# Performance work log

Measured on AMD Instinct MI355X. Metric: run time of the kernel, lower is better.

Reference implementation:

```python
import math
import jax, jax.numpy as jnp
import numpy as np

QUERY_DIM = 768
FEAT_DIM = 1024
HID_DIM = 768
OUT_DIM = 768
B, L, S, T = 32, 256, 64, 64


def _linear_params(key, fan_in, fan_out):
    kw, kb = jax.random.split(key)
    scale = 1.0 / math.sqrt(fan_in)
    W = jax.random.uniform(kw, (fan_in, fan_out), jnp.float32, -scale, scale)
    b = jax.random.uniform(kb, (fan_out,), jnp.float32, -scale, scale)
    return W, b


def setup_inputs() -> dict:
    key = jax.random.key(0)
    ks = jax.random.split(key, 7)
    query = jax.random.normal(ks[0], (B, L, QUERY_DIM), jnp.float32)
    src = jax.random.normal(ks[1], (B, S, FEAT_DIM), jnp.float32)
    trg = jax.random.normal(ks[2], (B, T, FEAT_DIM), jnp.float32)
    Wq, b_q = _linear_params(ks[3], QUERY_DIM, HID_DIM)
    Ws, b_s = _linear_params(ks[4], FEAT_DIM, HID_DIM)
    Wt, b_t = _linear_params(ks[5], FEAT_DIM, HID_DIM)
    Wo, b_o = _linear_params(ks[6], HID_DIM + QUERY_DIM, OUT_DIM)
    return {"query": query, "src": src, "trg": trg,
            "Wq": Wq, "b_q": b_q, "Ws": Ws, "b_s": b_s,
            "Wt": Wt, "b_t": b_t, "Wo": Wo, "b_o": b_o}


def reference(query, src, trg, Wq, b_q, Ws, b_s, Wt, b_t, Wo, b_o):
    # Projections (LinearAct with identity activation).
    q = query @ Wq + b_q          # (b, l, h)
    s_key = src @ Ws + b_s        # (b, s, h)
    t_key = trg @ Wt + b_t        # (b, t, h)
    # rel_key[b, t, s, h] = tanh(s_key[b, s, h] + t_key[b, t, h])
    rel_key = jnp.tanh(s_key[:, None, :, :] + t_key[:, :, None, :])  # (b, t, s, h)
    # Scores over combined (t, s) positions.
    weight = jnp.einsum('blk,btsk->blts', q, rel_key) / math.sqrt(HID_DIM)  # (b, l, t, s)
    b_, l_, t_, s_ = weight.shape
    weight = jax.nn.softmax(weight.reshape(b_, l_, t_ * s_), axis=-1).reshape(b_, l_, t_, s_)
    # Context: weighted sum of rel_key over (t, s).
    rel_ctx = jnp.einsum('blts,btsk->blk', weight, rel_key)  # (b, l, h)
    x = jnp.concatenate([query, rel_ctx], axis=-1)           # (b, l, h + q)
    return jax.nn.relu(x @ Wo + b_o)                          # (b, l, out)
```

## Files before the change

kernel.cpp:

```cpp
#include <hip/hip_runtime.h>
#include <math.h>


typedef __attribute__((ext_vector_type(8))) short bf16x8;
typedef __attribute__((ext_vector_type(4))) float f32x4;

__device__ __forceinline__ unsigned short f2bf(float f) {
    union { float f; unsigned u; } x; x.f = f;
    unsigned u = x.u;
    return (unsigned short)((u + 0x7fffu + ((u >> 16) & 1u)) >> 16);
}
__device__ __forceinline__ float bf2f(unsigned short h) {
    union { unsigned u; float f; } x; x.u = (unsigned)h << 16;
    return x.f;
}
__device__ __forceinline__ float tanh_fast(float x) {
    float e = __expf(2.0f * x);
    return 1.0f - 2.0f * __builtin_amdgcn_rcpf(1.0f + e);
}
__device__ __forceinline__ void async_copy16(void* lds, const void* g) {
    __builtin_amdgcn_global_load_lds(
        (const __attribute__((address_space(1))) unsigned int*)g,
        (__attribute__((address_space(3))) unsigned int*)lds,
        16, 0, 0);
}

template<bool OUT_BF16, bool RELU>
__global__ __launch_bounds__(256, 2) void gemm_bt_kernel(
    const unsigned short* __restrict__ A, const unsigned short* __restrict__ BT,
    void* __restrict__ Cout, const float* __restrict__ bias,
    int M, int N, int K, int lda, int ldb, int ldc)
{
    __shared__ unsigned short As[128 * 32];
    __shared__ unsigned short Bs[128 * 32];
    const int m0 = blockIdx.x * 128, n0 = blockIdx.y * 128;
    const int tid = threadIdx.x;
    const int lane = tid & 63, wid = tid >> 6;
    const int wr = wid >> 1, wc = wid & 1;
    const int r = lane & 15, g = lane >> 4;

    f32x4 acc[4][4] = {};

    for (int k0 = 0; k0 < K; k0 += 32) {
        __syncthreads();
        #pragma unroll
        for (int j = 0; j < 2; ++j) {
            int c = j * 256 + tid;
            int row = c >> 2, kc = (c & 3) * 8;
            async_copy16(&As[c * 8], A  + (size_t)(m0 + row) * lda + k0 + kc);
            async_copy16(&Bs[c * 8], BT + (size_t)(n0 + row) * ldb + k0 + kc);
        }
        asm volatile("s_waitcnt vmcnt(0)" ::: "memory");
        __syncthreads();

        bf16x8 af[4], bfr[4];
        #pragma unroll
        for (int m = 0; m < 4; ++m)
            af[m] = *(const bf16x8*)&As[(wr * 64 + m * 16 + r) * 32 + g * 8];
        #pragma unroll
        for (int n = 0; n < 4; ++n)
            bfr[n] = *(const bf16x8*)&Bs[(wc * 64 + n * 16 + r) * 32 + g * 8];
        #pragma unroll
        for (int m = 0; m < 4; ++m)
            #pragma unroll
            for (int n = 0; n < 4; ++n)
                acc[m][n] = __builtin_amdgcn_mfma_f32_16x16x32_bf16(
                    af[m], bfr[n], acc[m][n], 0, 0, 0);
    }

    float* Cf = (float*)Cout;
    unsigned short* Cb = (unsigned short*)Cout;
    #pragma unroll
    for (int n = 0; n < 4; ++n) {
        int col = n0 + wc * 64 + n * 16 + r;
        float bv = bias ? bias[col] : 0.0f;
        #pragma unroll
        for (int m = 0; m < 4; ++m) {
            int row0 = m0 + wr * 64 + m * 16 + g * 4;
            #pragma unroll
            for (int i = 0; i < 4; ++i) {
                float v = acc[m][n][i] + bv;
                if (RELU) v = fmaxf(v, 0.0f);
                size_t off = (size_t)(row0 + i) * ldc + col;
                if (OUT_BF16) Cb[off] = f2bf(v);
                else          Cf[off] = v;
            }
        }
    }
}

__global__ __launch_bounds__(256, 2) void scores_kernel(
    const unsigned short* __restrict__ qh,
    const float* __restrict__ s_key,
    const float* __restrict__ t_key,
    unsigned short* __restrict__ scores)
{
    __shared__ unsigned short As[128 * 32];
    __shared__ unsigned short Bs[128 * 32];
    __shared__ float Sk[64 * 32];
    __shared__ float Tk[64];

    const int b = blockIdx.z;
    const unsigned short* A = qh + (size_t)b * 256 * 768;
    const float* skp = s_key + (size_t)b * 64 * 768;
    const float* tkp = t_key + (size_t)b * 64 * 768;
    const int m0 = blockIdx.x * 128, n0 = blockIdx.y * 128;
    const int t0 = n0 >> 6;
    const int tid = threadIdx.x;
    const int lane = tid & 63, wid = tid >> 6;
    const int wr = wid >> 1, wc = wid & 1;
    const int r = lane & 15, g = lane >> 4;

    f32x4 acc[4][4] = {};

    for (int k0 = 0; k0 < 768; k0 += 32) {
        __syncthreads();
        if (tid < 64) Tk[tid] = tkp[(size_t)(t0 + (tid >> 5)) * 768 + k0 + (tid & 31)];
        #pragma unroll
        for (int j = 0; j < 2; ++j) {
            int c = j * 256 + tid;
            int row = c >> 2, kc = (c & 3) * 8;
            async_copy16(&As[c * 8], A + (size_t)(m0 + row) * 768 + k0 + kc);
            int s = c >> 3, k4 = (c & 7) * 4;
            async_copy16(&Sk[s * 32 + k4], skp + (size_t)s * 768 + k0 + k4);
        }
        asm volatile("s_waitcnt vmcnt(0)" ::: "memory");
        __syncthreads();

        #pragma unroll
        for (int j = 0; j < 2; ++j) {
            int c = j * 256 + tid;
            int n = c >> 2, kc = (c & 3) * 8;
            const float* sv = &Sk[(n & 63) * 32 + kc];
            const float* tv = &Tk[(n >> 6) * 32 + kc];
            bf16x8 o;
            #pragma unroll
            for (int e = 0; e < 8; ++e)
                o[e] = (short)f2bf(tanh_fast(sv[e] + tv[e]));
            *(bf16x8*)&Bs[n * 32 + kc] = o;
        }
        __syncthreads();

        bf16x8 af[4], bfr[4];
        #pragma unroll
        for (int m = 0; m < 4; ++m)
            af[m] = *(const bf16x8*)&As[(wr * 64 + m * 16 + r) * 32 + g * 8];
        #pragma unroll
        for (int n = 0; n < 4; ++n)
            bfr[n] = *(const bf16x8*)&Bs[(wc * 64 + n * 16 + r) * 32 + g * 8];
        #pragma unroll
        for (int m = 0; m < 4; ++m)
            #pragma unroll
            for (int n = 0; n < 4; ++n)
                acc[m][n] = __builtin_amdgcn_mfma_f32_16x16x32_bf16(
                    af[m], bfr[n], acc[m][n], 0, 0, 0);
    }

    unsigned short* C = scores + (size_t)b * 256 * 4096;
    #pragma unroll
    for (int n = 0; n < 4; ++n) {
        int col = n0 + wc * 64 + n * 16 + r;
        #pragma unroll
        for (int m = 0; m < 4; ++m) {
            int row0 = m0 + wr * 64 + m * 16 + g * 4;
            #pragma unroll
            for (int i = 0; i < 4; ++i)
                C[(size_t)(row0 + i) * 4096 + col] = f2bf(acc[m][n][i]);
        }
    }
}

__global__ __launch_bounds__(256, 2) void ctx_kernel(
    const unsigned short* __restrict__ w,
    const float* __restrict__ s_keyT,
    const float* __restrict__ t_keyT,
    unsigned short* __restrict__ xcat)
{
    __shared__ unsigned short As[128 * 32];
    __shared__ unsigned short Bs[128 * 32];
    __shared__ float SkT[128 * 32];
    __shared__ unsigned short TkTb[128 * 64];

    const int b = blockIdx.z;
    const unsigned short* A = w + (size_t)b * 256 * 4096;
    const float* skT = s_keyT + (size_t)b * 768 * 64;
    const float* tkT = t_keyT + (size_t)b * 768 * 64;
    const int m0 = blockIdx.x * 128, n0 = blockIdx.y * 128;
    const int tid = threadIdx.x;
    const int lane = tid & 63, wid = tid >> 6;
    const int wr = wid >> 1, wc = wid & 1;
    const int r = lane & 15, g = lane >> 4;

    for (int j = tid; j < 128 * 64; j += 256)
        TkTb[j] = f2bf(tkT[(size_t)n0 * 64 + j]);

    f32x4 acc[4][4] = {};

    for (int k0 = 0; k0 < 4096; k0 += 32) {
        const int t = k0 >> 6, s0 = k0 & 63;
        __syncthreads();
        #pragma unroll
        for (int j = 0; j < 2; ++j) {
            int c = j * 256 + tid;
            int row = c >> 2, kc = (c & 3) * 8;
            async_copy16(&As[c * 8], A + (size_t)(m0 + row) * 4096 + k0 + kc);
        }
        #pragma unroll
        for (int j = 0; j < 4; ++j) {
            int c = j * 256 + tid;
            int h = c >> 3, k4 = (c & 7) * 4;
            async_copy16(&SkT[h * 32 + k4], skT + (size_t)(n0 + h) * 64 + s0 + k4);
        }
        asm volatile("s_waitcnt vmcnt(0)" ::: "memory");
        __syncthreads();

        #pragma unroll
        for (int j = 0; j < 2; ++j) {
            int c = j * 256 + tid;
            int h = c >> 2, kc = (c & 3) * 8;
            const float* sv = &SkT[h * 32 + kc];
            float tval = bf2f(TkTb[h * 64 + t]);
            bf16x8 o;
            #pragma unroll
            for (int e = 0; e < 8; ++e)
                o[e] = (short)f2bf(tanh_fast(sv[e] + tval));
            *(bf16x8*)&Bs[h * 32 + kc] = o;
        }
        __syncthreads();

        bf16x8 af[4], bfr[4];
        #pragma unroll
        for (int m = 0; m < 4; ++m)
            af[m] = *(const bf16x8*)&As[(wr * 64 + m * 16 + r) * 32 + g * 8];
        #pragma unroll
        for (int n = 0; n < 4; ++n)
            bfr[n] = *(const bf16x8*)&Bs[(wc * 64 + n * 16 + r) * 32 + g * 8];
        #pragma unroll
        for (int m = 0; m < 4; ++m)
            #pragma unroll
            for (int n = 0; n < 4; ++n)
                acc[m][n] = __builtin_amdgcn_mfma_f32_16x16x32_bf16(
                    af[m], bfr[n], acc[m][n], 0, 0, 0);
    }

    unsigned short* C = xcat + (size_t)b * 256 * 1536 + 768;
    #pragma unroll
    for (int n = 0; n < 4; ++n) {
        int col = n0 + wc * 64 + n * 16 + r;
        #pragma unroll
        for (int m = 0; m < 4; ++m) {
            int row0 = m0 + wr * 64 + m * 16 + g * 4;
            #pragma unroll
            for (int i = 0; i < 4; ++i)
                C[(size_t)(row0 + i) * 1536 + col] = f2bf(acc[m][n][i]);
        }
    }
}

__global__ void cvt_bf16_kernel(const float* __restrict__ in,
                                unsigned short* __restrict__ out, int n4) {
    int i = blockIdx.x * 256 + threadIdx.x;
    if (i >= n4) return;
    float4 v = ((const float4*)in)[i];
    ushort4 o;
    o.x = f2bf(v.x); o.y = f2bf(v.y); o.z = f2bf(v.z); o.w = f2bf(v.w);
    ((ushort4*)out)[i] = o;
}

__global__ void cvt_query_kernel(const float* __restrict__ in,
                                 unsigned short* __restrict__ xcat) {
    int i = blockIdx.x * 256 + threadIdx.x;
    if (i >= 8192 * 192) return;
    int row = i / 192, c4 = (i % 192) * 4;
    float4 v = ((const float4*)in)[i];
    ushort4 o;
    o.x = f2bf(v.x); o.y = f2bf(v.y); o.z = f2bf(v.z); o.w = f2bf(v.w);
    *(ushort4*)&xcat[(size_t)row * 1536 + c4] = o;
}

__global__ void transpose_w_kernel(const float* __restrict__ in,
                                   unsigned short* __restrict__ out,
                                   int R, int C) {
    __shared__ float tile[64][65];
    const int r0 = blockIdx.y * 64, c0 = blockIdx.x * 64;
    const int tx = threadIdx.x & 63, ty = threadIdx.x >> 6;
    for (int i = ty; i < 64; i += 4)
        tile[i][tx] = in[(size_t)(r0 + i) * C + c0 + tx];
    __syncthreads();
    for (int i = ty; i < 64; i += 4)
        out[(size_t)(c0 + i) * R + r0 + tx] = f2bf(tile[tx][i]);
}

__global__ void transpose_sk_kernel(const float* __restrict__ in,
                                    float* __restrict__ out) {
    __shared__ float tile[64][65];
    const int b = blockIdx.y, c0 = blockIdx.x * 64;
    const float* src = in + (size_t)b * 64 * 768;
    float* dst = out + (size_t)b * 768 * 64;
    const int tx = threadIdx.x & 63, ty = threadIdx.x >> 6;
    for (int i = ty; i < 64; i += 4)
        tile[i][tx] = src[(size_t)i * 768 + c0 + tx];
    __syncthreads();
    for (int i = ty; i < 64; i += 4)
        dst[(size_t)(c0 + i) * 64 + tx] = tile[tx][i];
}

__global__ __launch_bounds__(256) void softmax_kernel(unsigned short* __restrict__ scores) {
    unsigned short* p = scores + (size_t)blockIdx.x * 4096;
    const int tid = threadIdx.x, lane = tid & 63, wid = tid >> 6;
    __shared__ float red[4];

    float v[16];
    {
        const bf16x8* p8 = (const bf16x8*)p;
        bf16x8 a = p8[tid * 2], c = p8[tid * 2 + 1];
        #pragma unroll
        for (int e = 0; e < 8; ++e) {
            v[e]     = bf2f((unsigned short)a[e]);
            v[8 + e] = bf2f((unsigned short)c[e]);
        }
    }
    float mx = v[0];
    #pragma unroll
    for (int e = 1; e < 16; ++e) mx = fmaxf(mx, v[e]);
    #pragma unroll
    for (int o = 32; o; o >>= 1) mx = fmaxf(mx, __shfl_xor(mx, o));
    if (lane == 0) red[wid] = mx;
    __syncthreads();
    mx = fmaxf(fmaxf(red[0], red[1]), fmaxf(red[2], red[3]));
    __syncthreads();

    const float scale = 0.03608439182435161f;
    float sum = 0.0f;
    #pragma unroll
    for (int e = 0; e < 16; ++e) {
        v[e] = __expf((v[e] - mx) * scale);
        sum += v[e];
    }
    #pragma unroll
    for (int o = 32; o; o >>= 1) sum += __shfl_xor(sum, o);
    if (lane == 0) red[wid] = sum;
    __syncthreads();
    sum = red[0] + red[1] + red[2] + red[3];
    const float inv = 1.0f / sum;

    bf16x8* p8 = (bf16x8*)p;
    #pragma unroll
    for (int j = 0; j < 2; ++j) {
        bf16x8 o;
        #pragma unroll
        for (int e = 0; e < 8; ++e)
            o[e] = (short)f2bf(v[j * 8 + e] * inv);
        p8[tid * 2 + j] = o;
    }
}

extern "C" void kernel_launch(void* const* d_in, const int* in_sizes, int n_in,
                              void* d_out, int out_size, void* d_ws, size_t ws_size,
                              hipStream_t stream) {
    const float* query = (const float*)d_in[0];
    const float* src   = (const float*)d_in[1];
    const float* trg   = (const float*)d_in[2];
    const float* Wq    = (const float*)d_in[3];
    const float* b_q   = (const float*)d_in[4];
    const float* Ws    = (const float*)d_in[5];
    const float* b_s   = (const float*)d_in[6];
    const float* Wt    = (const float*)d_in[7];
    const float* b_t   = (const float*)d_in[8];
    const float* Wo    = (const float*)d_in[9];
    const float* b_o   = (const float*)d_in[10];

    char* ws = (char*)d_ws;
    size_t off = 0;
    auto alloc = [&](size_t bytes) {
        void* p = ws + off;
        off += (bytes + 255) & ~(size_t)255;
        return p;
    };
    unsigned short* xcat   = (unsigned short*)alloc((size_t)8192 * 1536 * 2);
    unsigned short* srcbf  = (unsigned short*)alloc((size_t)2048 * 1024 * 2);
    unsigned short* trgbf  = (unsigned short*)alloc((size_t)2048 * 1024 * 2);
    unsigned short* WqT    = (unsigned short*)alloc((size_t)768 * 768 * 2);
    unsigned short* WsT    = (unsigned short*)alloc((size_t)768 * 1024 * 2);
    unsigned short* WtT    = (unsigned short*)alloc((size_t)768 * 1024 * 2);
    unsigned short* WoT    = (unsigned short*)alloc((size_t)768 * 1536 * 2);
    unsigned short* qh     = (unsigned short*)alloc((size_t)8192 * 768 * 2);
    float*          s_key  = (float*)alloc((size_t)2048 * 768 * 4);
    float*          t_key  = (float*)alloc((size_t)2048 * 768 * 4);
    float*          s_keyT = (float*)alloc((size_t)32 * 768 * 64 * 4);
    float*          t_keyT = (float*)alloc((size_t)32 * 768 * 64 * 4);
    unsigned short* scores = (unsigned short*)alloc((size_t)32 * 256 * 4096 * 2);

    cvt_query_kernel<<<6144, 256, 0, stream>>>(query, xcat);
    cvt_bf16_kernel<<<2048, 256, 0, stream>>>(src, srcbf, 524288);
    cvt_bf16_kernel<<<2048, 256, 0, stream>>>(trg, trgbf, 524288);

    transpose_w_kernel<<<dim3(12, 12), 256, 0, stream>>>(Wq, WqT, 768, 768);
    transpose_w_kernel<<<dim3(12, 16), 256, 0, stream>>>(Ws, WsT, 1024, 768);
    transpose_w_kernel<<<dim3(12, 16), 256, 0, stream>>>(Wt, WtT, 1024, 768);
    transpose_w_kernel<<<dim3(12, 24), 256, 0, stream>>>(Wo, WoT, 1536, 768);

    gemm_bt_kernel<true, false><<<dim3(64, 6), 256, 0, stream>>>(
        xcat, WqT, qh, b_q, 8192, 768, 768, 1536, 768, 768);
    gemm_bt_kernel<false, false><<<dim3(16, 6), 256, 0, stream>>>(
        srcbf, WsT, s_key, b_s, 2048, 768, 1024, 1024, 1024, 768);
    gemm_bt_kernel<false, false><<<dim3(16, 6), 256, 0, stream>>>(
        trgbf, WtT, t_key, b_t, 2048, 768, 1024, 1024, 1024, 768);

    transpose_sk_kernel<<<dim3(12, 32), 256, 0, stream>>>(s_key, s_keyT);
    transpose_sk_kernel<<<dim3(12, 32), 256, 0, stream>>>(t_key, t_keyT);

    scores_kernel<<<dim3(2, 32, 32), 256, 0, stream>>>(qh, s_key, t_key, scores);

    softmax_kernel<<<8192, 256, 0, stream>>>(scores);

    ctx_kernel<<<dim3(2, 6, 32), 256, 0, stream>>>(scores, s_keyT, t_keyT, xcat);

    gemm_bt_kernel<false, true><<<dim3(64, 6), 256, 0, stream>>>(
        xcat, WoT, d_out, b_o, 8192, 768, 1536, 1536, 1536, 768);
}
```

Baseline: 556.9 us.

## Materialize transposed bf16 rel_key and use batched GEMM for context

Adds a kernel that computes tanh(s_key + t_key) once and stores it in bf16, laid out as (h, t*s) per batch. The context step then runs as a batched GEMM of scores against that tensor, replacing ctx_kernel, which rebuilt the tanh values for every output tile. The gemm kernel gains per-batch stride arguments. The cost is a 200MB workspace write and read, and the fast path only runs when the workspace is large enough.

Result: no change. 554.8 us (-0.4%).

```diff
diff --git a/kernel.cpp b/kernel.cpp
--- a/kernel.cpp
+++ b/kernel.cpp
@@ -29,10 +29,14 @@
 __global__ __launch_bounds__(256, 2) void gemm_bt_kernel(
     const unsigned short* __restrict__ A, const unsigned short* __restrict__ BT,
     void* __restrict__ Cout, const float* __restrict__ bias,
-    int M, int N, int K, int lda, int ldb, int ldc)
+    int M, int N, int K, int lda, int ldb, int ldc,
+    long long sA, long long sB, long long sC)
 {
     __shared__ unsigned short As[128 * 32];
     __shared__ unsigned short Bs[128 * 32];
+    const int z = blockIdx.z;
+    A  += (long long)z * sA;
+    BT += (long long)z * sB;
     const int m0 = blockIdx.x * 128, n0 = blockIdx.y * 128;
     const int tid = threadIdx.x;
     const int lane = tid & 63, wid = tid >> 6;
@@ -70,6 +74,7 @@
 
     float* Cf = (float*)Cout;
     unsigned short* Cb = (unsigned short*)Cout;
+    const long long cbase = (long long)z * sC;
     #pragma unroll
     for (int n = 0; n < 4; ++n) {
         int col = n0 + wc * 64 + n * 16 + r;
@@ -81,7 +86,7 @@
             for (int i = 0; i < 4; ++i) {
                 float v = acc[m][n][i] + bv;
                 if (RELU) v = fmaxf(v, 0.0f);
-                size_t off = (size_t)(row0 + i) * ldc + col;
+                size_t off = (size_t)cbase + (size_t)(row0 + i) * ldc + col;
                 if (OUT_BF16) Cb[off] = f2bf(v);
                 else          Cf[off] = v;
             }
@@ -254,6 +259,29 @@
             for (int i = 0; i < 4; ++i)
                 C[(size_t)(row0 + i) * 1536 + col] = f2bf(acc[m][n][i]);
         }
+    }
+}
+
+__global__ __launch_bounds__(256) void relkT_kernel(
+    const float* __restrict__ s_key,
+    const float* __restrict__ t_key,
+    unsigned short* __restrict__ relkT)
+{
+    const int b = blockIdx.x >> 6, t = blockIdx.x & 63;
+    const float* sk = s_key + (size_t)b * 64 * 768;
+    const float* tk = t_key + ((size_t)b * 64 + t) * 768;
+    unsigned short* rkT = relkT + (size_t)b * 768 * 4096 + t * 64;
+    const int tx = threadIdx.x & 63, ty = threadIdx.x >> 6;
+    __shared__ float tile[64][65];
+    for (int h0 = 0; h0 < 768; h0 += 64) {
+        for (int s = ty; s < 64; s += 4)
+            tile[s][tx] = sk[(size_t)s * 768 + h0 + tx];
+        __syncthreads();
+        for (int h = ty; h < 64; h += 4) {
+            float tval = tk[h0 + h];
+            rkT[(size_t)(h0 + h) * 4096 + tx] = f2bf(tanh_fast(tile[tx][h] + tval));
+        }
+        __syncthreads();
     }
 }
 
@@ -387,9 +415,18 @@
     unsigned short* qh     = (unsigned short*)alloc((size_t)8192 * 768 * 2);
     float*          s_key  = (float*)alloc((size_t)2048 * 768 * 4);
     float*          t_key  = (float*)alloc((size_t)2048 * 768 * 4);
-    float*          s_keyT = (float*)alloc((size_t)32 * 768 * 64 * 4);
-    float*          t_keyT = (float*)alloc((size_t)32 * 768 * 64 * 4);
     unsigned short* scores = (unsigned short*)alloc((size_t)32 * 256 * 4096 * 2);
+
+    const bool fast = ws_size >= 340000000ULL;
+
+    unsigned short* relkT  = nullptr;
+    float* s_keyT = nullptr, * t_keyT = nullptr;
+    if (fast) {
+        relkT = (unsigned short*)alloc((size_t)32 * 768 * 4096 * 2);
+    } else {
+        s_keyT = (float*)alloc((size_t)32 * 768 * 64 * 4);
+        t_keyT = (float*)alloc((size_t)32 * 768 * 64 * 4);
+    }
 
     cvt_query_kernel<<<6144, 256, 0, stream>>>(query, xcat);
     cvt_bf16_kernel<<<2048, 256, 0, stream>>>(src, srcbf, 524288);
@@ -400,22 +437,33 @@
     transpose_w_kernel<<<dim3(12, 16), 256, 0, stream>>>(Wt, WtT, 1024, 768);
     transpose_w_kernel<<<dim3(12, 24), 256, 0, stream>>>(Wo, WoT, 1536, 768);
 
-    gemm_bt_kernel<true, false><<<dim3(64, 6), 256, 0, stream>>>(
-        xcat, WqT, qh, b_q, 8192, 768, 768, 1536, 768, 768);
-    gemm_bt_kernel<false, false><<<dim3(16, 6), 256, 0, stream>>>(
-        srcbf, WsT, s_key, b_s, 2048, 768, 1024, 1024, 1024, 768);
-    gemm_bt_kernel<false, false><<<dim3(16, 6), 256, 0, stream>>>(
-        trgbf, WtT, t_key, b_t, 2048, 768, 1024, 1024, 1024, 768);
-
-    transpose_sk_kernel<<<dim3(12, 32), 256, 0, stream>>>(s_key, s_keyT);
-    transpose_sk_kernel<<<dim3(12, 32), 256, 0, stream>>>(t_key, t_keyT);
+    gemm_bt_kernel<true, false><<<dim3(64, 6, 1), 256, 0, stream>>>(
+        xcat, WqT, qh, b_q, 8192, 768, 768, 1536, 768, 768, 0, 0, 0);
+    gemm_bt_kernel<false, false><<<dim3(16, 6, 1), 256, 0, stream>>>(
+        srcbf, WsT, s_key, b_s, 2048, 768, 1024, 1024, 1024, 768, 0, 0, 0);
+    gemm_bt_kernel<false, false><<<dim3(16, 6, 1), 256, 0, stream>>>(
+        trgbf, WtT, t_key, b_t, 2048, 768, 1024, 1024, 1024, 768, 0, 0, 0);
+
+    if (fast) {
+        relkT_kernel<<<2048, 256, 0, stream>>>(s_key, t_key, relkT);
+    } else {
+        transpose_sk_kernel<<<dim3(12, 32), 256, 0, stream>>>(s_key, s_keyT);
+        transpose_sk_kernel<<<dim3(12, 32), 256, 0, stream>>>(t_key, t_keyT);
+    }
 
     scores_kernel<<<dim3(2, 32, 32), 256, 0, stream>>>(qh, s_key, t_key, scores);
 
     softmax_kernel<<<8192, 256, 0, stream>>>(scores);
 
-    ctx_kernel<<<dim3(2, 6, 32), 256, 0, stream>>>(scores, s_keyT, t_keyT, xcat);
-
-    gemm_bt_kernel<false, true><<<dim3(64, 6), 256, 0, stream>>>(
-        xcat, WoT, d_out, b_o, 8192, 768, 1536, 1536, 1536, 768);
-}
+    if (fast) {
+        gemm_bt_kernel<true, false><<<dim3(2, 6, 32), 256, 0, stream>>>(
+            scores, relkT, xcat + 768, nullptr,
+            256, 768, 4096, 4096, 4096, 1536,
+            256LL * 4096, 768LL * 4096, 256LL * 1536);
+    } else {
+        ctx_kernel<<<dim3(2, 6, 32), 256, 0, stream>>>(scores, s_keyT, t_keyT, xcat);
+    }
+
+    gemm_bt_kernel<false, true><<<dim3(64, 6, 1), 256, 0, stream>>>(
+        xcat, WoT, d_out, b_o, 8192, 768, 1536, 1536, 1536, 768, 0, 0, 0);
+}
```

## Drop s/t key transposes; ctx kernel reads row-major keys via padded LDS

Applied to the files above, without the earlier changes.

Removes the two transpose_sk launches and their transposed buffers. ctx_kernel now stages a 64x128 slice of s_key in padded shared memory once per block and builds the tanh tile directly into a padded Bs (stride 40), reading t_key rows from global, which also drops one barrier per k-step. scores_kernel pads its Sk and Bs shared tiles to reduce bank conflicts and loads s_key with plain float4 loads instead of async copies. gemm_bt_kernel gains batch-stride arguments that are passed as zero and are unused.

Result: faster. 513.8 us (-7.7%).

```diff
diff --git a/kernel.cpp b/kernel.cpp
--- a/kernel.cpp
+++ b/kernel.cpp
@@ -29,10 +29,14 @@
 __global__ __launch_bounds__(256, 2) void gemm_bt_kernel(
     const unsigned short* __restrict__ A, const unsigned short* __restrict__ BT,
     void* __restrict__ Cout, const float* __restrict__ bias,
-    int M, int N, int K, int lda, int ldb, int ldc)
+    int M, int N, int K, int lda, int ldb, int ldc,
+    long long sA, long long sB, long long sC)
 {
     __shared__ unsigned short As[128 * 32];
     __shared__ unsigned short Bs[128 * 32];
+    const int z = blockIdx.z;
+    A  += (long long)z * sA;
+    BT += (long long)z * sB;
     const int m0 = blockIdx.x * 128, n0 = blockIdx.y * 128;
     const int tid = threadIdx.x;
     const int lane = tid & 63, wid = tid >> 6;
@@ -70,6 +74,7 @@
 
     float* Cf = (float*)Cout;
     unsigned short* Cb = (unsigned short*)Cout;
+    const long long cbase = (long long)z * sC;
     #pragma unroll
     for (int n = 0; n < 4; ++n) {
         int col = n0 + wc * 64 + n * 16 + r;
@@ -81,7 +86,7 @@
             for (int i = 0; i < 4; ++i) {
                 float v = acc[m][n][i] + bv;
                 if (RELU) v = fmaxf(v, 0.0f);
-                size_t off = (size_t)(row0 + i) * ldc + col;
+                size_t off = (size_t)cbase + (size_t)(row0 + i) * ldc + col;
                 if (OUT_BF16) Cb[off] = f2bf(v);
                 else          Cf[off] = v;
             }
@@ -96,9 +101,9 @@
     unsigned short* __restrict__ scores)
 {
     __shared__ unsigned short As[128 * 32];
-    __shared__ unsigned short Bs[128 * 32];
-    __shared__ float Sk[64 * 32];
-    __shared__ float Tk[64];
+    __shared__ unsigned short Bs[128 * 40];
+    __shared__ float Sk[64 * 36];
+    __shared__ float Tk[2 * 32];
 
     const int b = blockIdx.z;
     const unsigned short* A = qh + (size_t)b * 256 * 768;
@@ -121,8 +126,13 @@
             int c = j * 256 + tid;
             int row = c >> 2, kc = (c & 3) * 8;
             async_copy16(&As[c * 8], A + (size_t)(m0 + row) * 768 + k0 + kc);
-            int s = c >> 3, k4 = (c & 7) * 4;
-            async_copy16(&Sk[s * 32 + k4], skp + (size_t)s * 768 + k0 + k4);
+        }
+        {
+            int s = tid >> 2, c4 = (tid & 3) * 8;
+            float4 v0 = *(const float4*)&skp[(size_t)s * 768 + k0 + c4];
+            float4 v1 = *(const float4*)&skp[(size_t)s * 768 + k0 + c4 + 4];
+            *(float4*)&Sk[s * 36 + c4]     = v0;
+            *(float4*)&Sk[s * 36 + c4 + 4] = v1;
         }
         asm volatile("s_waitcnt vmcnt(0)" ::: "memory");
         __syncthreads();
@@ -131,13 +141,13 @@
         for (int j = 0; j < 2; ++j) {
             int c = j * 256 + tid;
             int n = c >> 2, kc = (c & 3) * 8;
-            const float* sv = &Sk[(n & 63) * 32 + kc];
+            const float* sv = &Sk[(n & 63) * 36 + kc];
             const float* tv = &Tk[(n >> 6) * 32 + kc];
             bf16x8 o;
             #pragma unroll
             for (int e = 0; e < 8; ++e)
                 o[e] = (short)f2bf(tanh_fast(sv[e] + tv[e]));
-            *(bf16x8*)&Bs[n * 32 + kc] = o;
+            *(bf16x8*)&Bs[n * 40 + kc] = o;
         }
         __syncthreads();
 
@@ -147,7 +157,7 @@
             af[m] = *(const bf16x8*)&As[(wr * 64 + m * 16 + r) * 32 + g * 8];
         #pragma unroll
         for (int n = 0; n < 4; ++n)
-            bfr[n] = *(const bf16x8*)&Bs[(wc * 64 + n * 16 + r) * 32 + g * 8];
+            bfr[n] = *(const bf16x8*)&Bs[(wc * 64 + n * 16 + r) * 40 + g * 8];
         #pragma unroll
         for (int m = 0; m < 4; ++m)
             #pragma unroll
@@ -172,29 +182,36 @@
 
 __global__ __launch_bounds__(256, 2) void ctx_kernel(
     const unsigned short* __restrict__ w,
-    const float* __restrict__ s_keyT,
-    const float* __restrict__ t_keyT,
+    const float* __restrict__ s_key,
+    const float* __restrict__ t_key,
     unsigned short* __restrict__ xcat)
 {
     __shared__ unsigned short As[128 * 32];
-    __shared__ unsigned short Bs[128 * 32];
-    __shared__ float SkT[128 * 32];
-    __shared__ unsigned short TkTb[128 * 64];
+    __shared__ unsigned short Bs[128 * 40];
+    __shared__ float Sk[64 * 132];
 
     const int b = blockIdx.z;
     const unsigned short* A = w + (size_t)b * 256 * 4096;
-    const float* skT = s_keyT + (size_t)b * 768 * 64;
-    const float* tkT = t_keyT + (size_t)b * 768 * 64;
+    const float* skp = s_key + (size_t)b * 64 * 768;
+    const float* tkp = t_key + (size_t)b * 64 * 768;
     const int m0 = blockIdx.x * 128, n0 = blockIdx.y * 128;
     const int tid = threadIdx.x;
     const int lane = tid & 63, wid = tid >> 6;
     const int wr = wid >> 1, wc = wid & 1;
     const int r = lane & 15, g = lane >> 4;
 
-    for (int j = tid; j < 128 * 64; j += 256)
-        TkTb[j] = f2bf(tkT[(size_t)n0 * 64 + j]);
+    #pragma unroll
+    for (int it = 0; it < 8; ++it) {
+        int idx = it * 256 + tid;
+        int s = idx >> 5, c4 = (idx & 31) * 4;
+        *(float4*)&Sk[s * 132 + c4] = *(const float4*)&skp[(size_t)s * 768 + n0 + c4];
+    }
+
+    const int sl = tid & 31;
+    const int hq = tid >> 5;
 
     f32x4 acc[4][4] = {};
+    __syncthreads();
 
     for (int k0 = 0; k0 < 4096; k0 += 32) {
         const int t = k0 >> 6, s0 = k0 & 63;
@@ -206,35 +223,40 @@
             async_copy16(&As[c * 8], A + (size_t)(m0 + row) * 4096 + k0 + kc);
         }
         #pragma unroll
-        for (int j = 0; j < 4; ++j) {
-            int c = j * 256 + tid;
-            int h = c >> 3, k4 = (c & 7) * 4;
-            async_copy16(&SkT[h * 32 + k4], skT + (size_t)(n0 + h) * 64 + s0 + k4);
+        for (int j = 0; j < 2; ++j) {
+            int h0 = (j * 8 + hq) * 8;
+            int s = s0 + sl;
+            float4 sa = *(const float4*)&Sk[s * 132 + h0];
+            float4 sb = *(const float4*)&Sk[s * 132 + h0 + 4];
+            float4 ta = *(const float4*)&tkp[(size_t)t * 768 + n0 + h0];
+            float4 tb = *(const float4*)&tkp[(size_t)t * 768 + n0 + h0 + 4];
+            unsigned short o0 = f2bf(tanh_fast(sa.x + ta.x));
+            unsigned short o1 = f2bf(tanh_fast(sa.y + ta.y));
+            unsigned short o2 = f2bf(tanh_fast(sa.z + ta.z));
+            unsigned short o3 = f2bf(tanh_fast(sa.w + ta.w));
+            unsigned short o4 = f2bf(tanh_fast(sb.x + tb.x));
+            unsigned short o5 = f2bf(tanh_fast(sb.y + tb.y));
+            unsigned short o6 = f2bf(tanh_fast(sb.z + tb.z));
+            unsigned short o7 = f2bf(tanh_fast(sb.w + tb.w));
+            Bs[(h0 + 0) * 40 + sl] = o0;
+            Bs[(h0 + 1) * 40 + sl] = o1;
+            Bs[(h0 + 2) * 40 + sl] = o2;
+            Bs[(h0 + 3) * 40 + sl] = o3;
+            Bs[(h0 + 4) * 40 + sl] = o4;
+            Bs[(h0 + 5) * 40 + sl] = o5;
+            Bs[(h0 + 6) * 40 + sl] = o6;
+            Bs[(h0 + 7) * 40 + sl] = o7;
         }
         asm volatile("s_waitcnt vmcnt(0)" ::: "memory");
         __syncthreads();
 
-        #pragma unroll
-        for (int j = 0; j < 2; ++j) {
-            int c = j * 256 + tid;
-            int h = c >> 2, kc = (c & 3) * 8;
-            const float* sv = &SkT[h * 32 + kc];
-            float tval = bf2f(TkTb[h * 64 + t]);
-            bf16x8 o;
-            #pragma unroll
-            for (int e = 0; e < 8; ++e)
-                o[e] = (short)f2bf(tanh_fast(sv[e] + tval));
-            *(bf16x8*)&Bs[h * 32 + kc] = o;
-        }
-        __syncthreads();
-
         bf16x8 af[4], bfr[4];
         #pragma unroll
         for (int m = 0; m < 4; ++m)
             af[m] = *(const bf16x8*)&As[(wr * 64 + m * 16 + r) * 32 + g * 8];
         #pragma unroll
         for (int n = 0; n < 4; ++n)
-            bfr[n] = *(const bf16x8*)&Bs[(wc * 64 + n * 16 + r) * 32 + g * 8];
+            bfr[n] = *(const bf16x8*)&Bs[(wc * 64 + n * 16 + r) * 40 + g * 8];
         #pragma unroll
         for (int m = 0; m < 4; ++m)
             #pragma unroll
@@ -289,20 +311,6 @@
     __syncthreads();
     for (int i = ty; i < 64; i += 4)
         out[(size_t)(c0 + i) * R + r0 + tx] = f2bf(tile[tx][i]);
-}
-
-__global__ void transpose_sk_kernel(const float* __restrict__ in,
-                                    float* __restrict__ out) {
-    __shared__ float tile[64][65];
-    const int b = blockIdx.y, c0 = blockIdx.x * 64;
-    const float* src = in + (size_t)b * 64 * 768;
-    float* dst = out + (size_t)b * 768 * 64;
-    const int tx = threadIdx.x & 63, ty = threadIdx.x >> 6;
-    for (int i = ty; i < 64; i += 4)
-        tile[i][tx] = src[(size_t)i * 768 + c0 + tx];
-    __syncthreads();
-    for (int i = ty; i < 64; i += 4)
-        dst[(size_t)(c0 + i) * 64 + tx] = tile[tx][i];
 }
 
 __global__ __launch_bounds__(256) void softmax_kernel(unsigned short* __restrict__ scores) {
@@ -387,8 +395,6 @@
     unsigned short* qh     = (unsigned short*)alloc((size_t)8192 * 768 * 2);
     float*          s_key  = (float*)alloc((size_t)2048 * 768 * 4);
     float*          t_key  = (float*)alloc((size_t)2048 * 768 * 4);
-    float*          s_keyT = (float*)alloc((size_t)32 * 768 * 64 * 4);
-    float*          t_keyT = (float*)alloc((size_t)32 * 768 * 64 * 4);
     unsigned short* scores = (unsigned short*)alloc((size_t)32 * 256 * 4096 * 2);
 
     cvt_query_kernel<<<6144, 256, 0, stream>>>(query, xcat);
@@ -400,22 +406,19 @@
     transpose_w_kernel<<<dim3(12, 16), 256, 0, stream>>>(Wt, WtT, 1024, 768);
     transpose_w_kernel<<<dim3(12, 24), 256, 0, stream>>>(Wo, WoT, 1536, 768);
 
-    gemm_bt_kernel<true, false><<<dim3(64, 6), 256, 0, stream>>>(
-        xcat, WqT, qh, b_q, 8192, 768, 768, 1536, 768, 768);
-    gemm_bt_kernel<false, false><<<dim3(16, 6), 256, 0, stream>>>(
-        srcbf, WsT, s_key, b_s, 2048, 768, 1024, 1024, 1024, 768);
-    gemm_bt_kernel<false, false><<<dim3(16, 6), 256, 0, stream>>>(
-        trgbf, WtT, t_key, b_t, 2048, 768, 1024, 1024, 1024, 768);
-
-    transpose_sk_kernel<<<dim3(12, 32), 256, 0, stream>>>(s_key, s_keyT);
-    transpose_sk_kernel<<<dim3(12, 32), 256, 0, stream>>>(t_key, t_keyT);
+    gemm_bt_kernel<true, false><<<dim3(64, 6, 1), 256, 0, stream>>>(
+        xcat, WqT, qh, b_q, 8192, 768, 768, 1536, 768, 768, 0, 0, 0);
+    gemm_bt_kernel<false, false><<<dim3(16, 6, 1), 256, 0, stream>>>(
+        srcbf, WsT, s_key, b_s, 2048, 768, 1024, 1024, 1024, 768, 0, 0, 0);
+    gemm_bt_kernel<false, false><<<dim3(16, 6, 1), 256, 0, stream>>>(
+        trgbf, WtT, t_key, b_t, 2048, 768, 1024, 1024, 1024, 768, 0, 0, 0);
 
     scores_kernel<<<dim3(2, 32, 32), 256, 0, stream>>>(qh, s_key, t_key, scores);
 
     softmax_kernel<<<8192, 256, 0, stream>>>(scores);
 
-    ctx_kernel<<<dim3(2, 6, 32), 256, 0, stream>>>(scores, s_keyT, t_keyT, xcat);
-
-    gemm_bt_kernel<false, true><<<dim3(64, 6), 256, 0, stream>>>(
-        xcat, WoT, d_out, b_o, 8192, 768, 1536, 1536, 1536, 768);
-}
+    ctx_kernel<<<dim3(2, 6, 32), 256, 0, stream>>>(scores, s_key, t_key, xcat);
+
+    gemm_bt_kernel<false, true><<<dim3(64, 6, 1), 256, 0, stream>>>(
+        xcat, WoT, d_out, b_o, 8192, 768, 1536, 1536, 1536, 768, 0, 0, 0);
+}
```
